# Performance work log

Hardware: AMD Instinct MI355X
Metric: run time of the kernel (lower is better)

Reference implementation:

```python
import jax, jax.numpy as jnp
import numpy as np

N_NODES = 100000


def gcn_conv(x, row, col, W, b, n_nodes):
    # PyG GCNConv: add self-loops, symmetric normalization, linear, scatter-add, bias
    deg = jnp.zeros((n_nodes,), x.dtype).at[col].add(1.0)
    dinv = jnp.where(deg > 0, jax.lax.rsqrt(deg), 0.0)
    norm = dinv[row] * dinv[col]                      # [E+N]
    h = x @ W                                         # [N, out]
    msg = h[row] * norm[:, None]                      # [E+N, out]
    out = jax.ops.segment_sum(msg, col, num_segments=n_nodes)
    return out + b


def setup_inputs() -> dict:
    key = jax.random.key(0)
    ks = jax.random.split(key, 8)
    E = 1600000
    edge_index = jax.random.randint(ks[0], (2, E), 0, N_NODES, dtype=jnp.int64)
    node_features = jax.random.normal(ks[1], (N_NODES, 16), dtype=jnp.float32)
    W1 = jax.random.normal(ks[2], (16, 32), dtype=jnp.float32) * 0.25
    b1 = jnp.zeros((32,), jnp.float32)
    W2 = jax.random.normal(ks[3], (32, 16), dtype=jnp.float32) * 0.18
    b2 = jnp.zeros((16,), jnp.float32)
    fc_W = jax.random.normal(ks[4], (16, 1), dtype=jnp.float32) * 0.25
    fc_b = jnp.zeros((1,), jnp.float32)
    return {"edge_index": edge_index, "node_features": node_features,
            "W1": W1, "b1": b1, "W2": W2, "b2": b2, "fc_W": fc_W, "fc_b": fc_b}


def reference(edge_index, node_features, W1, b1, W2, b2, fc_W, fc_b):
    n = node_features.shape[0]
    loops = jnp.arange(n, dtype=edge_index.dtype)
    row = jnp.concatenate([edge_index[0], loops])     # sources (with self-loops)
    col = jnp.concatenate([edge_index[1], loops])     # targets (with self-loops)
    x = jax.nn.relu(gcn_conv(node_features, row, col, W1, b1, n))
    # F.dropout with training=False is identity (inference)
    x = jax.nn.relu(gcn_conv(x, row, col, W2, b2, n))
    return x @ fc_W + fc_b
```

## Files before the change

### kernel.cpp

```cpp
#include <hip/hip_runtime.h>
#include <hip/hip_fp16.h>


constexpr int NN  = 100000;
constexpr int FIN = 16;
constexpr int FH  = 32;
constexpr int FO  = 16;

constexpr int BK      = 256;
constexpr int NBUCKET = (NN + BK - 1) / BK;
constexpr int CHUNK   = 8192;
constexpr int CAP     = 5632;

static __device__ __forceinline__ int pack2(float a, float b) {
    __half2 t = __float22half2_rn(make_float2(a, b));
    return *reinterpret_cast<int*>(&t);
}
static __device__ __forceinline__ float2 unpack2(int v) {
    __half2 t = *reinterpret_cast<__half2*>(&v);
    return __half22float2(t);
}

__global__ void init_kernel(int* __restrict__ bcursor,
                            __half* __restrict__ g1, __half* __restrict__ g2) {
    int b = blockIdx.x * blockDim.x + threadIdx.x;
    if (b < NBUCKET) bcursor[b] = b * CAP;
    if (b < 4) ((int4*)(g1 + (long long)NN * FH))[b] = make_int4(0, 0, 0, 0);
    else if (b < 6) ((int4*)(g2 + (long long)NN * FO))[b - 4] = make_int4(0, 0, 0, 0);
}

__global__ __launch_bounds__(512) void bucket_fill_kernel(
        const int* __restrict__ row, const int* __restrict__ col,
        int* __restrict__ bcursor, int* __restrict__ srow, int E) {
    __shared__ int bcnt[NBUCKET];
    __shared__ int bcur[NBUCKET];
    int t = threadIdx.x;
    int e0 = blockIdx.x * CHUNK;
    int m = E - e0; if (m > CHUNK) m = CHUNK;
    for (int b = t; b < NBUCKET; b += 512) bcnt[b] = 0;
    __syncthreads();
    for (int i = t; i < m; i += 512)
        atomicAdd(&bcnt[col[e0 + i] >> 8], 1);
    __syncthreads();
    for (int b = t; b < NBUCKET; b += 512) {
        int v = bcnt[b];
        bcur[b] = v ? atomicAdd(&bcursor[b], v) : 0;
    }
    __syncthreads();
    for (int i = t; i < m; i += 512) {
        int c = col[e0 + i];
        int r = row[e0 + i];
        int p = atomicAdd(&bcur[c >> 8], 1);
        srow[p] = ((c & (BK - 1)) << 17) | r;
    }
}

__global__ __launch_bounds__(512) void bucket_sort_mm1_kernel(
        const int* __restrict__ bcursor, int* __restrict__ srow,
        int* __restrict__ off, int* __restrict__ cnt, float* __restrict__ dinv,
        const float* __restrict__ x, const float* __restrict__ W1,
        __half* __restrict__ g1, int n) {
    __shared__ int ebuf[CAP];
    __shared__ int sorted[CAP];
    __shared__ int cnt2[BK];
    __shared__ float sdi[BK];
    __shared__ int wsum[4];
    __shared__ int wbase[4];
    __shared__ int Mtot;
    __shared__ float w1[FIN * FH];
    int t = threadIdx.x;
    for (int i = t; i < FIN * FH; i += 512) w1[i] = W1[i];
    int lo = blockIdx.x << 8;
    int nodes = n - lo; if (nodes > BK) nodes = BK;
    int s0 = blockIdx.x * CAP;
    int m = bcursor[blockIdx.x] - s0;
    if (m > CAP) m = CAP;
    if (m < 0)  m = 0;
    for (int i = t; i < m; i += 512) ebuf[i] = srow[s0 + i];
    if (t < BK) cnt2[t] = 0;
    __syncthreads();
    for (int i = t; i < m; i += 512) atomicAdd(&cnt2[ebuf[i] >> 17], 1);
    __syncthreads();
    int v = 0, pv = 0, s = 0, excl = 0;
    if (t < BK) {
        v  = cnt2[t];
        pv = (v + 3) & ~3;
        s  = pv;
        #pragma unroll
        for (int d = 1; d < 64; d <<= 1) {
            int u = __shfl_up(s, d, 64);
            if ((t & 63) >= d) s += u;
        }
        if ((t & 63) == 63) wsum[t >> 6] = s;
    }
    __syncthreads();
    if (t < 4) {
        int b = 0;
        for (int k = 0; k < t; k++) b += wsum[k];
        wbase[t] = b;
    }
    __syncthreads();
    if (t < BK) {
        excl = s + wbase[t >> 6] - pv;
        cnt2[t] = excl;
        float di = rsqrtf((float)v + 1.0f);
        sdi[t] = di;
        if (t < nodes) {
            off[lo + t]  = s0 + excl;
            cnt[lo + t]  = v;
            dinv[lo + t] = di;
        }
        if (t == BK - 1) Mtot = excl + pv;
    }
    __syncthreads();
    for (int i = t; i < m; i += 512) {
        int pvv = ebuf[i];
        int p = atomicAdd(&cnt2[pvv >> 17], 1);
        sorted[p] = pvv & 0x1FFFF;
    }
    __syncthreads();
    if (t < BK) {
        for (int p = excl + v; p < excl + pv; p++) sorted[p] = NN;
    }
    __syncthreads();
    int M = Mtot; if (M > CAP) M = CAP;
    for (int i = t; i < M; i += 512) srow[s0 + i] = sorted[i];
    int lane = t >> 8;
    int nd0  = t & 255;
    if (nd0 < nodes) {
        int nd = lo + nd0;
        float di = sdi[nd0];
        float xi[FIN];
        const float4* xv = (const float4*)(x + (long long)nd * FIN);
        #pragma unroll
        for (int i = 0; i < FIN / 4; i++) {
            float4 vv = xv[i];
            xi[4*i] = vv.x; xi[4*i+1] = vv.y; xi[4*i+2] = vv.z; xi[4*i+3] = vv.w;
        }
        float h[16];
        #pragma unroll
        for (int j = 0; j < 16; j++) h[j] = 0.f;
        const float* wl = w1 + lane * 16;
        #pragma unroll
        for (int i = 0; i < FIN; i++) {
            float xs = xi[i];
            #pragma unroll
            for (int j = 0; j < 16; j++) h[j] += xs * wl[i * FH + j];
        }
        int4* gv = (int4*)(g1 + (long long)nd * FH) + lane * 2;
        gv[0] = make_int4(pack2(h[0]*di,  h[1]*di),  pack2(h[2]*di,  h[3]*di),
                          pack2(h[4]*di,  h[5]*di),  pack2(h[6]*di,  h[7]*di));
        gv[1] = make_int4(pack2(h[8]*di,  h[9]*di),  pack2(h[10]*di, h[11]*di),
                          pack2(h[12]*di, h[13]*di), pack2(h[14]*di, h[15]*di));
    }
}

constexpr int XS = 36;
__global__ __launch_bounds__(256) void gather_mm2_kernel(
        const int* __restrict__ off, const int* __restrict__ cnt,
        const int* __restrict__ srow, const __half* __restrict__ g1,
        const float* __restrict__ dinv, const float* __restrict__ b1,
        const float* __restrict__ W2, __half* __restrict__ g2, int n) {
    __shared__ float xs[64 * XS];
    __shared__ float w[FH * FO];
    __shared__ float bb[FH];
    int t = threadIdx.x;
    for (int i = t; i < FH * FO; i += 256) w[i] = W2[i];
    if (t < FH) bb[t] = b1[t];
    int nl = t >> 2;
    int q = t & 3;
    int node = blockIdx.x * 64 + nl;
    bool live = node < n;
    float acc[8] = {0.f,0.f,0.f,0.f,0.f,0.f,0.f,0.f};
    float di = 0.f;
    if (live) {
        di = dinv[node];
        {
            int4 raw = ((const int4*)(g1 + (long long)node * FH))[q];
            float2 f0 = unpack2(raw.x), f1 = unpack2(raw.y);
            float2 f2 = unpack2(raw.z), f3 = unpack2(raw.w);
            acc[0] = f0.x; acc[1] = f0.y; acc[2] = f1.x; acc[3] = f1.y;
            acc[4] = f2.x; acc[5] = f2.y; acc[6] = f3.x; acc[7] = f3.y;
        }
        int s = off[node];
        int m = cnt[node];
        for (int i = 0; i < m; i += 4) {
            int4 ix = *(const int4*)(srow + s + i);
            int4 ra = ((const int4*)(g1 + (long long)ix.x * FH))[q];
            int4 rb = ((const int4*)(g1 + (long long)ix.y * FH))[q];
            int4 rc = ((const int4*)(g1 + (long long)ix.z * FH))[q];
            int4 rd = ((const int4*)(g1 + (long long)ix.w * FH))[q];
            float2 u;
            u = unpack2(ra.x); acc[0] += u.x; acc[1] += u.y;
            u = unpack2(ra.y); acc[2] += u.x; acc[3] += u.y;
            u = unpack2(ra.z); acc[4] += u.x; acc[5] += u.y;
            u = unpack2(ra.w); acc[6] += u.x; acc[7] += u.y;
            u = unpack2(rb.x); acc[0] += u.x; acc[1] += u.y;
            u = unpack2(rb.y); acc[2] += u.x; acc[3] += u.y;
            u = unpack2(rb.z); acc[4] += u.x; acc[5] += u.y;
            u = unpack2(rb.w); acc[6] += u.x; acc[7] += u.y;
            u = unpack2(rc.x); acc[0] += u.x; acc[1] += u.y;
            u = unpack2(rc.y); acc[2] += u.x; acc[3] += u.y;
            u = unpack2(rc.z); acc[4] += u.x; acc[5] += u.y;
            u = unpack2(rc.w); acc[6] += u.x; acc[7] += u.y;
            u = unpack2(rd.x); acc[0] += u.x; acc[1] += u.y;
            u = unpack2(rd.y); acc[2] += u.x; acc[3] += u.y;
            u = unpack2(rd.z); acc[4] += u.x; acc[5] += u.y;
            u = unpack2(rd.w); acc[6] += u.x; acc[7] += u.y;
        }
    }
    __syncthreads();
    if (live) {
        float* xr = xs + nl * XS + 8 * q;
        #pragma unroll
        for (int j = 0; j < 8; j++) {
            float a = acc[j] * di + bb[8*q + j];
            xr[j] = a > 0.f ? a : 0.f;
        }
    }
    __syncthreads();
    if (live) {
        const float* xr = xs + nl * XS;
        int k0 = 4 * q;
        float o0 = 0.f, o1 = 0.f, o2 = 0.f, o3 = 0.f;
        #pragma unroll
        for (int j = 0; j < FH; j++) {
            float xj = xr[j];
            const float* wr = w + j * FO + k0;
            o0 += xj * wr[0];
            o1 += xj * wr[1];
            o2 += xj * wr[2];
            o3 += xj * wr[3];
        }
        ((int2*)(g2 + (long long)node * FO))[q] =
            make_int2(pack2(o0 * di, o1 * di), pack2(o2 * di, o3 * di));
    }
}

__global__ __launch_bounds__(256) void gather_fc_kernel(
        const int* __restrict__ off, const int* __restrict__ cnt,
        const int* __restrict__ srow, const __half* __restrict__ g2,
        const float* __restrict__ dinv, const float* __restrict__ b2,
        const float* __restrict__ fcW, const float* __restrict__ fcb,
        float* __restrict__ out, int n) {
    __shared__ float w[FO];
    __shared__ float bb[FO];
    __shared__ float fb;
    int t = threadIdx.x;
    if (t < FO) { w[t] = fcW[t]; bb[t] = b2[t]; }
    if (t == 0) fb = fcb[0];
    __syncthreads();
    int node = blockIdx.x * 128 + (t >> 1);
    int q = t & 1;
    if (node >= n) return;
    float di = dinv[node];
    float acc[8];
    {
        int4 raw = ((const int4*)(g2 + (long long)node * FO))[q];
        float2 f0 = unpack2(raw.x), f1 = unpack2(raw.y);
        float2 f2 = unpack2(raw.z), f3 = unpack2(raw.w);
        acc[0] = f0.x; acc[1] = f0.y; acc[2] = f1.x; acc[3] = f1.y;
        acc[4] = f2.x; acc[5] = f2.y; acc[6] = f3.x; acc[7] = f3.y;
    }
    int s = off[node];
    int m = cnt[node];
    for (int i = 0; i < m; i += 4) {
        int4 ix = *(const int4*)(srow + s + i);
        int4 ra = ((const int4*)(g2 + (long long)ix.x * FO))[q];
        int4 rb = ((const int4*)(g2 + (long long)ix.y * FO))[q];
        int4 rc = ((const int4*)(g2 + (long long)ix.z * FO))[q];
        int4 rd = ((const int4*)(g2 + (long long)ix.w * FO))[q];
        float2 u;
        u = unpack2(ra.x); acc[0] += u.x; acc[1] += u.y;
        u = unpack2(ra.y); acc[2] += u.x; acc[3] += u.y;
        u = unpack2(ra.z); acc[4] += u.x; acc[5] += u.y;
        u = unpack2(ra.w); acc[6] += u.x; acc[7] += u.y;
        u = unpack2(rb.x); acc[0] += u.x; acc[1] += u.y;
        u = unpack2(rb.y); acc[2] += u.x; acc[3] += u.y;
        u = unpack2(rb.z); acc[4] += u.x; acc[5] += u.y;
        u = unpack2(rb.w); acc[6] += u.x; acc[7] += u.y;
        u = unpack2(rc.x); acc[0] += u.x; acc[1] += u.y;
        u = unpack2(rc.y); acc[2] += u.x; acc[3] += u.y;
        u = unpack2(rc.z); acc[4] += u.x; acc[5] += u.y;
        u = unpack2(rc.w); acc[6] += u.x; acc[7] += u.y;
        u = unpack2(rd.x); acc[0] += u.x; acc[1] += u.y;
        u = unpack2(rd.y); acc[2] += u.x; acc[3] += u.y;
        u = unpack2(rd.z); acc[4] += u.x; acc[5] += u.y;
        u = unpack2(rd.w); acc[6] += u.x; acc[7] += u.y;
    }
    float p = 0.f;
    #pragma unroll
    for (int j = 0; j < 8; j++) {
        float a = acc[j] * di + bb[8*q + j];
        p += (a > 0.f ? a : 0.f) * w[8*q + j];
    }
    p += __shfl_down(p, 1, 2);
    if (q == 0) out[node] = p + fb;
}

extern "C" void kernel_launch(void* const* d_in, const int* in_sizes, int n_in,
                              void* d_out, int out_size, void* d_ws, size_t ws_size,
                              hipStream_t stream) {
    const int*   edge = (const int*)d_in[0];
    const float* x    = (const float*)d_in[1];
    const float* W1   = (const float*)d_in[2];
    const float* b1   = (const float*)d_in[3];
    const float* W2   = (const float*)d_in[4];
    const float* b2   = (const float*)d_in[5];
    const float* fcW  = (const float*)d_in[6];
    const float* fcb  = (const float*)d_in[7];
    float* out = (float*)d_out;

    const int E = in_sizes[0] / 2;
    const int n = NN;
    const int* row = edge;
    const int* col = edge + E;

    const size_t nA = (size_t)((n + 127) & ~127);
    char* wsb = (char*)d_ws;
    int*   cnt     = (int*)wsb;
    int*   off     = cnt + nA;
    float* dinv    = (float*)(off + nA);
    int*   bcursor = (int*)(dinv + nA);
    int*   srow    = bcursor + 512;
    int*   srowEnd = srow + (size_t)(NBUCKET + 1) * CAP;
    __half* g1     = (__half*)srowEnd;
    __half* g2     = g1 + (size_t)(n + 1) * FH;

    const int nChunkBlocks = (E + CHUNK - 1) / CHUNK;

    init_kernel<<<2, 256, 0, stream>>>(bcursor, g1, g2);
    bucket_fill_kernel<<<nChunkBlocks, 512, 0, stream>>>(row, col, bcursor, srow, E);
    bucket_sort_mm1_kernel<<<NBUCKET, 512, 0, stream>>>(bcursor, srow, off, cnt, dinv, x, W1, g1, n);
    gather_mm2_kernel<<<(n + 63) / 64, 256, 0, stream>>>(off, cnt, srow, g1, dinv, b1, W2, g2, n);
    gather_fc_kernel<<<(n + 127) / 128, 256, 0, stream>>>(off, cnt, srow, g2, dinv, b2, fcW, fcb, out, n);
}
```

Before: 145.5 us.

## Drop init kernel, widen bucket blocks to 1024, prefetch indices in gathers

Replaces the init kernel with a memset of the bucket cursors, which now hold relative counts, and moves zeroing of the padding rows into the sort kernel. The bucket fill and sort kernels run 1024 threads per block, so the layer-1 matmul gives each thread 8 output columns instead of 16. Both gather kernels now unroll 8 neighbours per iteration and prefetch the next index vectors to hide latency. The goal is to save one launch and expose more memory-level parallelism, at the cost of more registers and a more complex tail.

```diff
diff --git a/kernel.cpp b/kernel.cpp
--- a/kernel.cpp
+++ b/kernel.cpp
@@ -21,15 +21,7 @@
     return __half22float2(t);
 }
 
-__global__ void init_kernel(int* __restrict__ bcursor,
-                            __half* __restrict__ g1, __half* __restrict__ g2) {
-    int b = blockIdx.x * blockDim.x + threadIdx.x;
-    if (b < NBUCKET) bcursor[b] = b * CAP;
-    if (b < 4) ((int4*)(g1 + (long long)NN * FH))[b] = make_int4(0, 0, 0, 0);
-    else if (b < 6) ((int4*)(g2 + (long long)NN * FO))[b - 4] = make_int4(0, 0, 0, 0);
-}
-
-__global__ __launch_bounds__(512) void bucket_fill_kernel(
+__global__ __launch_bounds__(1024) void bucket_fill_kernel(
         const int* __restrict__ row, const int* __restrict__ col,
         int* __restrict__ bcursor, int* __restrict__ srow, int E) {
     __shared__ int bcnt[NBUCKET];
@@ -37,17 +29,17 @@
     int t = threadIdx.x;
     int e0 = blockIdx.x * CHUNK;
     int m = E - e0; if (m > CHUNK) m = CHUNK;
-    for (int b = t; b < NBUCKET; b += 512) bcnt[b] = 0;
-    __syncthreads();
-    for (int i = t; i < m; i += 512)
+    for (int b = t; b < NBUCKET; b += 1024) bcnt[b] = 0;
+    __syncthreads();
+    for (int i = t; i < m; i += 1024)
         atomicAdd(&bcnt[col[e0 + i] >> 8], 1);
     __syncthreads();
-    for (int b = t; b < NBUCKET; b += 512) {
+    for (int b = t; b < NBUCKET; b += 1024) {
         int v = bcnt[b];
-        bcur[b] = v ? atomicAdd(&bcursor[b], v) : 0;
-    }
-    __syncthreads();
-    for (int i = t; i < m; i += 512) {
+        bcur[b] = v ? (b * CAP + atomicAdd(&bcursor[b], v)) : 0;
+    }
+    __syncthreads();
+    for (int i = t; i < m; i += 1024) {
         int c = col[e0 + i];
         int r = row[e0 + i];
         int p = atomicAdd(&bcur[c >> 8], 1);
@@ -55,11 +47,11 @@
     }
 }
 
-__global__ __launch_bounds__(512) void bucket_sort_mm1_kernel(
+__global__ __launch_bounds__(1024) void bucket_sort_mm1_kernel(
         const int* __restrict__ bcursor, int* __restrict__ srow,
         int* __restrict__ off, int* __restrict__ cnt, float* __restrict__ dinv,
         const float* __restrict__ x, const float* __restrict__ W1,
-        __half* __restrict__ g1, int n) {
+        __half* __restrict__ g1, __half* __restrict__ g2, int n) {
     __shared__ int ebuf[CAP];
     __shared__ int sorted[CAP];
     __shared__ int cnt2[BK];
@@ -69,17 +61,21 @@
     __shared__ int Mtot;
     __shared__ float w1[FIN * FH];
     int t = threadIdx.x;
-    for (int i = t; i < FIN * FH; i += 512) w1[i] = W1[i];
+    for (int i = t; i < FIN * FH; i += 1024) w1[i] = W1[i];
+    if (blockIdx.x == 0 && t < 6) {
+        if (t < 4) ((int4*)(g1 + (long long)NN * FH))[t] = make_int4(0, 0, 0, 0);
+        else       ((int4*)(g2 + (long long)NN * FO))[t - 4] = make_int4(0, 0, 0, 0);
+    }
     int lo = blockIdx.x << 8;
     int nodes = n - lo; if (nodes > BK) nodes = BK;
     int s0 = blockIdx.x * CAP;
-    int m = bcursor[blockIdx.x] - s0;
+    int m = bcursor[blockIdx.x];
     if (m > CAP) m = CAP;
     if (m < 0)  m = 0;
-    for (int i = t; i < m; i += 512) ebuf[i] = srow[s0 + i];
+    for (int i = t; i < m; i += 1024) ebuf[i] = srow[s0 + i];
     if (t < BK) cnt2[t] = 0;
     __syncthreads();
-    for (int i = t; i < m; i += 512) atomicAdd(&cnt2[ebuf[i] >> 17], 1);
+    for (int i = t; i < m; i += 1024) atomicAdd(&cnt2[ebuf[i] >> 17], 1);
     __syncthreads();
     int v = 0, pv = 0, s = 0, excl = 0;
     if (t < BK) {
@@ -113,7 +109,7 @@
         if (t == BK - 1) Mtot = excl + pv;
     }
     __syncthreads();
-    for (int i = t; i < m; i += 512) {
+    for (int i = t; i < m; i += 1024) {
         int pvv = ebuf[i];
         int p = atomicAdd(&cnt2[pvv >> 17], 1);
         sorted[p] = pvv & 0x1FFFF;
@@ -124,7 +120,7 @@
     }
     __syncthreads();
     int M = Mtot; if (M > CAP) M = CAP;
-    for (int i = t; i < M; i += 512) srow[s0 + i] = sorted[i];
+    for (int i = t; i < M; i += 1024) srow[s0 + i] = sorted[i];
     int lane = t >> 8;
     int nd0  = t & 255;
     if (nd0 < nodes) {
@@ -137,23 +133,28 @@
             float4 vv = xv[i];
             xi[4*i] = vv.x; xi[4*i+1] = vv.y; xi[4*i+2] = vv.z; xi[4*i+3] = vv.w;
         }
-        float h[16];
-        #pragma unroll
-        for (int j = 0; j < 16; j++) h[j] = 0.f;
-        const float* wl = w1 + lane * 16;
+        float h[8];
+        #pragma unroll
+        for (int j = 0; j < 8; j++) h[j] = 0.f;
+        const float* wl = w1 + lane * 8;
         #pragma unroll
         for (int i = 0; i < FIN; i++) {
             float xs = xi[i];
             #pragma unroll
-            for (int j = 0; j < 16; j++) h[j] += xs * wl[i * FH + j];
-        }
-        int4* gv = (int4*)(g1 + (long long)nd * FH) + lane * 2;
-        gv[0] = make_int4(pack2(h[0]*di,  h[1]*di),  pack2(h[2]*di,  h[3]*di),
-                          pack2(h[4]*di,  h[5]*di),  pack2(h[6]*di,  h[7]*di));
-        gv[1] = make_int4(pack2(h[8]*di,  h[9]*di),  pack2(h[10]*di, h[11]*di),
-                          pack2(h[12]*di, h[13]*di), pack2(h[14]*di, h[15]*di));
-    }
-}
+            for (int j = 0; j < 8; j++) h[j] += xs * wl[i * FH + j];
+        }
+        ((int4*)(g1 + (long long)nd * FH))[lane] =
+            make_int4(pack2(h[0]*di, h[1]*di), pack2(h[2]*di, h[3]*di),
+                      pack2(h[4]*di, h[5]*di), pack2(h[6]*di, h[7]*di));
+    }
+}
+
+#define ACC_ROW(R)                                          \
+    { float2 u;                                             \
+      u = unpack2((R).x); acc[0] += u.x; acc[1] += u.y;     \
+      u = unpack2((R).y); acc[2] += u.x; acc[3] += u.y;     \
+      u = unpack2((R).z); acc[4] += u.x; acc[5] += u.y;     \
+      u = unpack2((R).w); acc[6] += u.x; acc[7] += u.y; }
 
 constexpr int XS = 36;
 __global__ __launch_bounds__(256) void gather_mm2_kernel(
@@ -184,29 +185,39 @@
         }
         int s = off[node];
         int m = cnt[node];
-        for (int i = 0; i < m; i += 4) {
-            int4 ix = *(const int4*)(srow + s + i);
-            int4 ra = ((const int4*)(g1 + (long long)ix.x * FH))[q];
-            int4 rb = ((const int4*)(g1 + (long long)ix.y * FH))[q];
-            int4 rc = ((const int4*)(g1 + (long long)ix.z * FH))[q];
-            int4 rd = ((const int4*)(g1 + (long long)ix.w * FH))[q];
-            float2 u;
-            u = unpack2(ra.x); acc[0] += u.x; acc[1] += u.y;
-            u = unpack2(ra.y); acc[2] += u.x; acc[3] += u.y;
-            u = unpack2(ra.z); acc[4] += u.x; acc[5] += u.y;
-            u = unpack2(ra.w); acc[6] += u.x; acc[7] += u.y;
-            u = unpack2(rb.x); acc[0] += u.x; acc[1] += u.y;
-            u = unpack2(rb.y); acc[2] += u.x; acc[3] += u.y;
-            u = unpack2(rb.z); acc[4] += u.x; acc[5] += u.y;
-            u = unpack2(rb.w); acc[6] += u.x; acc[7] += u.y;
-            u = unpack2(rc.x); acc[0] += u.x; acc[1] += u.y;
-            u = unpack2(rc.y); acc[2] += u.x; acc[3] += u.y;
-            u = unpack2(rc.z); acc[4] += u.x; acc[5] += u.y;
-            u = unpack2(rc.w); acc[6] += u.x; acc[7] += u.y;
-            u = unpack2(rd.x); acc[0] += u.x; acc[1] += u.y;
-            u = unpack2(rd.y); acc[2] += u.x; acc[3] += u.y;
-            u = unpack2(rd.z); acc[4] += u.x; acc[5] += u.y;
-            u = unpack2(rd.w); acc[6] += u.x; acc[7] += u.y;
+        if (m > 0) {
+            int4 ixA = *(const int4*)(srow + s);
+            int4 ixB = *(const int4*)(srow + s + 4);
+            int i = 0;
+            for (; i + 8 < m; i += 8) {
+                int4 ixA2 = *(const int4*)(srow + s + i + 8);
+                int4 ixB2 = *(const int4*)(srow + s + i + 12);
+                int4 ra = ((const int4*)(g1 + (long long)ixA.x * FH))[q];
+                int4 rb = ((const int4*)(g1 + (long long)ixA.y * FH))[q];
+                int4 rc = ((const int4*)(g1 + (long long)ixA.z * FH))[q];
+                int4 rd = ((const int4*)(g1 + (long long)ixA.w * FH))[q];
+                int4 re = ((const int4*)(g1 + (long long)ixB.x * FH))[q];
+                int4 rf = ((const int4*)(g1 + (long long)ixB.y * FH))[q];
+                int4 rg = ((const int4*)(g1 + (long long)ixB.z * FH))[q];
+                int4 rh = ((const int4*)(g1 + (long long)ixB.w * FH))[q];
+                ACC_ROW(ra); ACC_ROW(rb); ACC_ROW(rc); ACC_ROW(rd);
+                ACC_ROW(re); ACC_ROW(rf); ACC_ROW(rg); ACC_ROW(rh);
+                ixA = ixA2; ixB = ixB2;
+            }
+            {
+                int4 ra = ((const int4*)(g1 + (long long)ixA.x * FH))[q];
+                int4 rb = ((const int4*)(g1 + (long long)ixA.y * FH))[q];
+                int4 rc = ((const int4*)(g1 + (long long)ixA.z * FH))[q];
+                int4 rd = ((const int4*)(g1 + (long long)ixA.w * FH))[q];
+                ACC_ROW(ra); ACC_ROW(rb); ACC_ROW(rc); ACC_ROW(rd);
+            }
+            if (i + 4 < m) {
+                int4 ra = ((const int4*)(g1 + (long long)ixB.x * FH))[q];
+                int4 rb = ((const int4*)(g1 + (long long)ixB.y * FH))[q];
+                int4 rc = ((const int4*)(g1 + (long long)ixB.z * FH))[q];
+                int4 rd = ((const int4*)(g1 + (long long)ixB.w * FH))[q];
+                ACC_ROW(ra); ACC_ROW(rb); ACC_ROW(rc); ACC_ROW(rd);
+            }
         }
     }
     __syncthreads();
@@ -264,29 +275,39 @@
     }
     int s = off[node];
     int m = cnt[node];
-    for (int i = 0; i < m; i += 4) {
-        int4 ix = *(const int4*)(srow + s + i);
-        int4 ra = ((const int4*)(g2 + (long long)ix.x * FO))[q];
-        int4 rb = ((const int4*)(g2 + (long long)ix.y * FO))[q];
-        int4 rc = ((const int4*)(g2 + (long long)ix.z * FO))[q];
-        int4 rd = ((const int4*)(g2 + (long long)ix.w * FO))[q];
-        float2 u;
-        u = unpack2(ra.x); acc[0] += u.x; acc[1] += u.y;
-        u = unpack2(ra.y); acc[2] += u.x; acc[3] += u.y;
-        u = unpack2(ra.z); acc[4] += u.x; acc[5] += u.y;
-        u = unpack2(ra.w); acc[6] += u.x; acc[7] += u.y;
-        u = unpack2(rb.x); acc[0] += u.x; acc[1] += u.y;
-        u = unpack2(rb.y); acc[2] += u.x; acc[3] += u.y;
-        u = unpack2(rb.z); acc[4] += u.x; acc[5] += u.y;
-        u = unpack2(rb.w); acc[6] += u.x; acc[7] += u.y;
-        u = unpack2(rc.x); acc[0] += u.x; acc[1] += u.y;
-        u = unpack2(rc.y); acc[2] += u.x; acc[3] += u.y;
-        u = unpack2(rc.z); acc[4] += u.x; acc[5] += u.y;
-        u = unpack2(rc.w); acc[6] += u.x; acc[7] += u.y;
-        u = unpack2(rd.x); acc[0] += u.x; acc[1] += u.y;
-        u = unpack2(rd.y); acc[2] += u.x; acc[3] += u.y;
-        u = unpack2(rd.z); acc[4] += u.x; acc[5] += u.y;
-        u = unpack2(rd.w); acc[6] += u.x; acc[7] += u.y;
+    if (m > 0) {
+        int4 ixA = *(const int4*)(srow + s);
+        int4 ixB = *(const int4*)(srow + s + 4);
+        int i = 0;
+        for (; i + 8 < m; i += 8) {
+            int4 ixA2 = *(const int4*)(srow + s + i + 8);
+            int4 ixB2 = *(const int4*)(srow + s + i + 12);
+            int4 ra = ((const int4*)(g2 + (long long)ixA.x * FO))[q];
+            int4 rb = ((const int4*)(g2 + (long long)ixA.y * FO))[q];
+            int4 rc = ((const int4*)(g2 + (long long)ixA.z * FO))[q];
+            int4 rd = ((const int4*)(g2 + (long long)ixA.w * FO))[q];
+            int4 re = ((const int4*)(g2 + (long long)ixB.x * FO))[q];
+            int4 rf = ((const int4*)(g2 + (long long)ixB.y * FO))[q];
+            int4 rg = ((const int4*)(g2 + (long long)ixB.z * FO))[q];
+            int4 rh = ((const int4*)(g2 + (long long)ixB.w * FO))[q];
+            ACC_ROW(ra); ACC_ROW(rb); ACC_ROW(rc); ACC_ROW(rd);
+            ACC_ROW(re); ACC_ROW(rf); ACC_ROW(rg); ACC_ROW(rh);
+            ixA = ixA2; ixB = ixB2;
+        }
+        {
+            int4 ra = ((const int4*)(g2 + (long long)ixA.x * FO))[q];
+            int4 rb = ((const int4*)(g2 + (long long)ixA.y * FO))[q];
+            int4 rc = ((const int4*)(g2 + (long long)ixA.z * FO))[q];
+            int4 rd = ((const int4*)(g2 + (long long)ixA.w * FO))[q];
+            ACC_ROW(ra); ACC_ROW(rb); ACC_ROW(rc); ACC_ROW(rd);
+        }
+        if (i + 4 < m) {
+            int4 ra = ((const int4*)(g2 + (long long)ixB.x * FO))[q];
+            int4 rb = ((const int4*)(g2 + (long long)ixB.y * FO))[q];
+            int4 rc = ((const int4*)(g2 + (long long)ixB.z * FO))[q];
+            int4 rd = ((const int4*)(g2 + (long long)ixB.w * FO))[q];
+            ACC_ROW(ra); ACC_ROW(rb); ACC_ROW(rc); ACC_ROW(rd);
+        }
     }
     float p = 0.f;
     #pragma unroll
@@ -329,9 +350,9 @@
 
     const int nChunkBlocks = (E + CHUNK - 1) / CHUNK;
 
-    init_kernel<<<2, 256, 0, stream>>>(bcursor, g1, g2);
-    bucket_fill_kernel<<<nChunkBlocks, 512, 0, stream>>>(row, col, bcursor, srow, E);
-    bucket_sort_mm1_kernel<<<NBUCKET, 512, 0, stream>>>(bcursor, srow, off, cnt, dinv, x, W1, g1, n);
+    hipMemsetAsync(bcursor, 0, 512 * sizeof(int), stream);
+    bucket_fill_kernel<<<nChunkBlocks, 1024, 0, stream>>>(row, col, bcursor, srow, E);
+    bucket_sort_mm1_kernel<<<NBUCKET, 1024, 0, stream>>>(bcursor, srow, off, cnt, dinv, x, W1, g1, g2, n);
     gather_mm2_kernel<<<(n + 63) / 64, 256, 0, stream>>>(off, cnt, srow, g1, dinv, b1, W2, g2, n);
     gather_fc_kernel<<<(n + 127) / 128, 256, 0, stream>>>(off, cnt, srow, g2, dinv, b2, fcW, fcb, out, n);
 }
```

Result: faster. 138.0 us (-5.2%).
